# Kernel tuning notes

Measured on AMD Instinct MI355X. Metric: run time of the kernel, lower is better.

## Reference

```python
import jax, jax.numpy as jnp
import numpy as np

H = 16  # hidden_dim
EPS = 1e-5


def _lstm_layer(x, W_ih, W_hh, b_ih, b_hh):
    # x: [B,T,D_in] -> [B,T,H]; PyTorch gate order i,f,g,o
    B = x.shape[0]
    xg = jnp.einsum('btd,gd->btg', x, W_ih) + (b_ih + b_hh)  # [B,T,4H]

    def step(carry, xt):
        h, c = carry
        gates = xt + h @ W_hh.T
        i, f, g, o = jnp.split(gates, 4, axis=-1)
        c = jax.nn.sigmoid(f) * c + jax.nn.sigmoid(i) * jnp.tanh(g)
        h = jax.nn.sigmoid(o) * jnp.tanh(c)
        return (h, c), h

    h0 = jnp.zeros((B, H), x.dtype)
    _, hs = jax.lax.scan(step, (h0, h0), jnp.swapaxes(xg, 0, 1))  # [T,B,H]
    return jnp.swapaxes(hs, 0, 1)


def setup_inputs() -> dict:
    key = jax.random.key(0)
    ks = jax.random.split(key, 20)
    B, T, D, O = 256, 2048, 57, 4
    x = jax.random.normal(ks[0], (B, T, D), dtype=jnp.float32)
    lengths = jnp.maximum(jnp.sort(jax.random.randint(ks[1], (B,), 1, T + 1))[::-1], 1)
    s = 1.0 / np.sqrt(H)
    u = lambda k, shp: jax.random.uniform(k, shp, jnp.float32, -s, s)
    inp = {'x': x, 'lengths': lengths}
    dims_in = [D, H, H]
    for l in range(3):
        inp[f'W_ih{l}'] = u(ks[2 + 4 * l], (4 * H, dims_in[l]))
        inp[f'W_hh{l}'] = u(ks[3 + 4 * l], (4 * H, H))
        inp[f'b_ih{l}'] = u(ks[4 + 4 * l], (4 * H,))
        inp[f'b_hh{l}'] = u(ks[5 + 4 * l], (4 * H,))
    inp['bn_gamma'] = jnp.ones((H,), jnp.float32)
    inp['bn_beta'] = jnp.zeros((H,), jnp.float32)
    inp['fc_w'] = u(ks[14], (O, H))
    inp['fc_b'] = u(ks[15], (O,))
    return inp


def reference(x, lengths, W_ih0, W_hh0, b_ih0, b_hh0, W_ih1, W_hh1, b_ih1, b_hh1,
              W_ih2, W_hh2, b_ih2, b_hh2, bn_gamma, bn_beta, fc_w, fc_b):
    B, T, _ = x.shape
    h = x
    for W_ih, W_hh, b_ih, b_hh in ((W_ih0, W_hh0, b_ih0, b_hh0),
                                    (W_ih1, W_hh1, b_ih1, b_hh1),
                                    (W_ih2, W_hh2, b_ih2, b_hh2)):
        h = _lstm_layer(h, W_ih, W_hh, b_ih, b_hh)
    # pad_packed_sequence: zero out positions past each sequence length
    mask = (jnp.arange(T)[None, :] < lengths[:, None])[:, :, None].astype(h.dtype)
    h = h * mask  # [B,T,H]
    # BatchNorm1d (training mode) over (batch,time) per channel, incl. padding zeros
    mean = jnp.mean(h, axis=(0, 1))
    var = jnp.mean((h - mean) ** 2, axis=(0, 1))
    norm = (h - mean) * jax.lax.rsqrt(var + EPS) * bn_gamma + bn_beta
    return norm @ fc_w.T + fc_b  # [B,T,4]
```

## Files before the change

kernel.cpp:

```cpp
#include <hip/hip_runtime.h>
#include <math.h>

#define TT 2048
#define BBATCH 256
#define DDIM 57
#define NROWS (BBATCH*TT)
#define NF 524288.0f
#define U 8
#define G 4
#define NBUF 8
#define XROWS 64

#define K1 (-1.4426950408889634f)
#define K2 (-2.8853900817779268f)

__device__ __forceinline__ float bcastl(float v, int k) {
  return __uint_as_float((unsigned)__builtin_amdgcn_readlane((int)__float_as_uint(v), k));
}
__device__ __forceinline__ float rcpf(float x) { return __builtin_amdgcn_rcpf(x); }
__device__ __forceinline__ float exp2f_(float x) { return __builtin_amdgcn_exp2f(x); }

template<int PAT>
__device__ __forceinline__ float quadb(float v) {
  return __int_as_float(__builtin_amdgcn_update_dpp(0, __float_as_int(v), PAT, 0xF, 0xF, true));
}

__global__ __launch_bounds__(256) void xg0_gemm_k(
    const float* __restrict__ x, const float* __restrict__ Wih,
    const float* __restrict__ bih, const float* __restrict__ bhh,
    float* __restrict__ xg0)
{
  const int tid = threadIdx.x;
  const int l   = tid & 63;
  const int w   = tid >> 6;
  const int g   = (l & 3) * 16 + (l >> 2);
  const float fac = ((l & 3) == 2) ? K2 : K1;

  __shared__ __align__(16) float xs[XROWS][60];

  float wv[60];
  #pragma unroll
  for (int d = 0; d < 60; ++d) wv[d] = (d < DDIM) ? fac * Wih[g*DDIM + d] : 0.f;
  const float bias = fac * (bih[g] + bhh[g]);

  const int rbase = blockIdx.x * XROWS;
  const float4* xsrc = (const float4*)(x + (size_t)rbase * DDIM);
  #pragma unroll
  for (int it = 0; it < 4; ++it) {
    int i = tid + it*256;
    if (i < 912) {
      float4 v = xsrc[i];
      int f0 = 4*i;
      int r0 = f0/57, d0 = f0 - r0*57;            xs[r0][d0] = v.x;
      int f1 = f0+1, r1 = f1/57, d1 = f1 - r1*57; xs[r1][d1] = v.y;
      int f2 = f0+2, r2 = f2/57, d2 = f2 - r2*57; xs[r2][d2] = v.z;
      int f3 = f0+3, r3 = f3/57, d3 = f3 - r3*57; xs[r3][d3] = v.w;
    }
  }
  if (tid < 192) {
    int r = tid/3, c = 57 + (tid - 3*r);
    xs[r][c] = 0.f;
  }
  __syncthreads();

  #pragma unroll
  for (int rr = 0; rr < 16; ++rr) {
    const int r = w*16 + rr;
    const float4* xr = (const float4*)&xs[r][0];
    float a0 = bias, a1 = 0.f, a2 = 0.f, a3 = 0.f;
    #pragma unroll
    for (int i = 0; i < 15; ++i) {
      float4 v = xr[i];
      a0 += wv[4*i]   * v.x;
      a1 += wv[4*i+1] * v.y;
      a2 += wv[4*i+2] * v.z;
      a3 += wv[4*i+3] * v.w;
    }
    xg0[(size_t)(rbase + r)*64 + l] = (a0 + a1) + (a2 + a3);
  }
}

__global__ __launch_bounds__(192, 1) void lstm_scan_pipe_k(
    const float* __restrict__ xg0,
    const int*   __restrict__ lengths,
    const float* __restrict__ Whh0,
    const float* __restrict__ Wih1, const float* __restrict__ Whh1,
    const float* __restrict__ bih1, const float* __restrict__ bhh1,
    const float* __restrict__ Wih2, const float* __restrict__ Whh2,
    const float* __restrict__ bih2, const float* __restrict__ bhh2,
    float* __restrict__ h2buf, float* __restrict__ partial)
{
  const int tid  = threadIdx.x;
  const int wave = tid >> 6;
  const int lane = tid & 63;
  const int gt   = lane & 3;
  const int ch   = lane >> 2;
  const int g    = gt*16 + ch;
  const int b    = blockIdx.x;
  const int len  = lengths[b];
  const bool isg = (gt == 2);
  const float fac = isg ? K2 : K1;
  const float mg = isg ? (2.f*K2) : 1.f;
  const float ag = isg ? (-K2)    : 0.f;

  __shared__ float lds_h0[NBUF][U][16];
  __shared__ float lds_h1[NBUF][U][16];

  float wa[16], wb[16];
  float bias = 0.f;
  if (wave == 0) {
    #pragma unroll
    for (int k = 0; k < 16; ++k) { wb[k] = fac * Whh0[g*16 + k]; wa[k] = 0.f; }
  } else if (wave == 1) {
    #pragma unroll
    for (int k = 0; k < 16; ++k) { wa[k] = fac * Wih1[g*16 + k]; wb[k] = fac * Whh1[g*16 + k]; }
    bias = fac * (bih1[g] + bhh1[g]);
  } else {
    #pragma unroll
    for (int k = 0; k < 16; ++k) { wa[k] = fac * Wih2[g*16 + k]; wb[k] = fac * Whh2[g*16 + k]; }
    bias = fac * (bih2[g] + bhh2[g]);
  }

  float hs = 0.f, csK = 0.f;
  float sum = 0.f, sq = 0.f;
  const int base = b*TT*64 + lane;
  float* __restrict__ h2row = h2buf + (size_t)b*TT*16;

  auto lstm_update = [&](float dot) {
    float s   = rcpf(1.f + exp2f_(dot));
    float act = fmaf(s, mg, ag);
    float gi = quadb<0x00>(act);
    float gf = quadb<0x55>(act);
    float gg = quadb<0xAA>(act);
    float go = quadb<0xFF>(act);
    float go2 = go + go;
    csK = fmaf(gf, csK, gg * gi);
    float r = rcpf(1.f + exp2f_(csK));
    hs = fmaf(go2, r, -go);
  };
  auto owndot = [&](float seed) {
    float hb[16];
    #pragma unroll
    for (int k = 0; k < 16; ++k) hb[k] = bcastl(hs, 4*k);
    float a0 = seed, a1 = 0.f, a2 = 0.f, a3 = 0.f;
    #pragma unroll
    for (int k = 0; k < 16; k += 4) {
      a0 += wb[k]   * hb[k];
      a1 += wb[k+1] * hb[k+1];
      a2 += wb[k+2] * hb[k+2];
      a3 += wb[k+3] * hb[k+3];
    }
    return (a0 + a1) + (a2 + a3);
  };
  auto indot = [&](const float* hin) {
    float a0 = bias, a1 = 0.f, a2 = 0.f, a3 = 0.f;
    #pragma unroll
    for (int k = 0; k < 16; k += 4) {
      a0 += wa[k]   * hin[k];
      a1 += wa[k+1] * hin[k+1];
      a2 += wa[k+2] * hin[k+2];
      a3 += wa[k+3] * hin[k+3];
    }
    return (a0 + a1) + (a2 + a3);
  };

  const int NS = (len + U - 1) / U;
  const int E  = (NS + 2*G - 1) / G + 1;

  float cur[U], nxt[U];
  if (wave == 0) {
    #pragma unroll
    for (int j = 0; j < U; ++j) cur[j] = xg0[base + j*64];
    #pragma unroll
    for (int j = 0; j < U; ++j) {
      int ip = U + j; ip = ip > TT-1 ? TT-1 : ip;
      nxt[j] = xg0[base + ip*64];
    }
  }

  for (int e = 0; e < E; ++e) {
    #pragma unroll 1
    for (int q = 0; q < G; ++q) {
      const int tw = G*e + q;
      if (wave == 0) {
        const int t = tw;
        if (t < NS) {
          const int p = t & (NBUF-1);
          float ld[U];
          #pragma unroll
          for (int j = 0; j < U; ++j) {
            int ip = (t + 2)*U + j; ip = ip > TT-1 ? TT-1 : ip;
            ld[j] = xg0[base + ip*64];
          }
          #pragma unroll
          for (int j = 0; j < U; ++j) {
            lstm_update(owndot(cur[j]));
            if (gt == 0) lds_h0[p][j][ch] = hs;
          }
          #pragma unroll
          for (int j = 0; j < U; ++j) { cur[j] = nxt[j]; nxt[j] = ld[j]; }
        }
      } else if (wave == 1) {
        const int t = tw - G;
        if (t >= 0 && t < NS) {
          const int p = t & (NBUF-1);
          float xin[U];
          #pragma unroll
          for (int j = 0; j < U; ++j) {
            const float4* hp = (const float4*)&lds_h0[p][j][0];
            float4 h0v = hp[0], h1v = hp[1], h2v = hp[2], h3v = hp[3];
            float hin[16] = {h0v.x,h0v.y,h0v.z,h0v.w, h1v.x,h1v.y,h1v.z,h1v.w,
                             h2v.x,h2v.y,h2v.z,h2v.w, h3v.x,h3v.y,h3v.z,h3v.w};
            xin[j] = indot(hin);
          }
          #pragma unroll
          for (int j = 0; j < U; ++j) {
            lstm_update(owndot(xin[j]));
            if (gt == 0) lds_h1[p][j][ch] = hs;
          }
        }
      } else {
        const int t = tw - 2*G;
        if (t >= 0 && t < NS) {
          const int p = t & (NBUF-1);
          float xin[U];
          #pragma unroll
          for (int j = 0; j < U; ++j) {
            const float4* hp = (const float4*)&lds_h1[p][j][0];
            float4 h0v = hp[0], h1v = hp[1], h2v = hp[2], h3v = hp[3];
            float hin[16] = {h0v.x,h0v.y,h0v.z,h0v.w, h1v.x,h1v.y,h1v.z,h1v.w,
                             h2v.x,h2v.y,h2v.z,h2v.w, h3v.x,h3v.y,h3v.z,h3v.w};
            xin[j] = indot(hin);
          }
          #pragma unroll
          for (int j = 0; j < U; ++j) {
            lstm_update(owndot(xin[j]));
            const int ts = t*U + j;
            if (ts < len) {
              if (gt == 0) h2row[ts*16 + ch] = hs;
              sum += hs; sq += hs*hs;
            }
          }
        }
      }
    }
    __syncthreads();
  }

  for (int idx = len*16 + tid; idx < TT*16; idx += 192)
    h2row[idx] = 0.f;

  if (wave == 2 && gt == 0) {
    partial[b*32 + ch]      = sum;
    partial[b*32 + 16 + ch] = sq;
  }
}

__global__ __launch_bounds__(256) void prep_k(
    const float* __restrict__ partial,
    const float* __restrict__ gamma, const float* __restrict__ beta,
    const float* __restrict__ fcw, const float* __restrict__ fcb,
    float* __restrict__ coef)
{
  const int tid = threadIdx.x;
  const int c = tid & 31, chunk = tid >> 5;
  float acc = 0.f;
  #pragma unroll 8
  for (int bb = 0; bb < 32; ++bb)
    acc += partial[(chunk*32 + bb)*32 + c];
  __shared__ float red[8][32];
  red[chunk][c] = acc;
  __syncthreads();
  if (tid < 32) {
    float tot = 0.f;
    #pragma unroll
    for (int k = 0; k < 8; ++k) tot += red[k][tid];
    red[0][tid] = tot;
  }
  __syncthreads();
  if (tid < 64) {
    const int o = tid >> 4, c2 = tid & 15;
    const float inv_n = 1.0f / NF;
    float mean = red[0][c2] * inv_n;
    float var  = red[0][16 + c2] * inv_n - mean*mean;
    float s  = gamma[c2] * rsqrtf(var + 1e-5f);
    float tb = beta[c2] - mean * s;
    float woc = fcw[o*16 + c2];
    coef[tid] = s * woc;
    float term = tb * woc;
    #pragma unroll
    for (int off = 1; off < 16; off <<= 1) term += __shfl_xor(term, off, 16);
    if (c2 == 0) coef[64 + o] = fcb[o] + term;
  }
}

__global__ __launch_bounds__(256) void finalize_k(
    const float* __restrict__ h2buf, const float* __restrict__ coef,
    float* __restrict__ out)
{
  const int r = blockIdx.x * 256 + threadIdx.x;
  const float4* hp = (const float4*)(h2buf + (size_t)r * 16);
  float4 v0 = hp[0], v1 = hp[1], v2 = hp[2], v3 = hp[3];
  float hv[16] = {v0.x,v0.y,v0.z,v0.w, v1.x,v1.y,v1.z,v1.w,
                  v2.x,v2.y,v2.z,v2.w, v3.x,v3.y,v3.z,v3.w};
  float4 o4;
  float* op = &o4.x;
  #pragma unroll
  for (int o = 0; o < 4; ++o) {
    float a = coef[64 + o];
    #pragma unroll
    for (int c = 0; c < 16; ++c) a += coef[o*16 + c] * hv[c];
    op[o] = a;
  }
  ((float4*)out)[r] = o4;
}

extern "C" void kernel_launch(void* const* d_in, const int* in_sizes, int n_in,
                              void* d_out, int out_size, void* d_ws, size_t ws_size,
                              hipStream_t stream)
{
  const float* x     = (const float*)d_in[0];
  const int* lengths = (const int*)d_in[1];
  const float* W_ih0 = (const float*)d_in[2];
  const float* W_hh0 = (const float*)d_in[3];
  const float* b_ih0 = (const float*)d_in[4];
  const float* b_hh0 = (const float*)d_in[5];
  const float* W_ih1 = (const float*)d_in[6];
  const float* W_hh1 = (const float*)d_in[7];
  const float* b_ih1 = (const float*)d_in[8];
  const float* b_hh1 = (const float*)d_in[9];
  const float* W_ih2 = (const float*)d_in[10];
  const float* W_hh2 = (const float*)d_in[11];
  const float* b_ih2 = (const float*)d_in[12];
  const float* b_hh2 = (const float*)d_in[13];
  const float* gamma = (const float*)d_in[14];
  const float* beta  = (const float*)d_in[15];
  const float* fcw   = (const float*)d_in[16];
  const float* fcb   = (const float*)d_in[17];
  float* out = (float*)d_out;

  float* ws      = (float*)d_ws;
  float* xg0     = ws;
  float* h2      = ws + 33554432;
  float* partial = ws + 33554432 + 8388608;
  float* coef    = partial + 8192;

  hipLaunchKernelGGL(xg0_gemm_k, dim3(NROWS/XROWS), dim3(256), 0, stream,
                     x, W_ih0, b_ih0, b_hh0, xg0);
  hipLaunchKernelGGL(lstm_scan_pipe_k, dim3(256), dim3(192), 0, stream,
                     xg0, lengths, W_hh0, W_ih1, W_hh1, b_ih1, b_hh1,
                     W_ih2, W_hh2, b_ih2, b_hh2, h2, partial);
  hipLaunchKernelGGL(prep_k, dim3(1), dim3(256), 0, stream,
                     partial, gamma, beta, fcw, fcb, coef);
  hipLaunchKernelGGL(finalize_k, dim3(2048), dim3(256), 0, stream, h2, coef, out);
}
```

Before: 646.5 us.

## Fuse LSTM scan, batchnorm stats, and FC epilogue via cooperative grid sync

Merges the scan kernel, the stats-reduction kernel and the finalize kernel into one cooperative launch. Layer-2 hidden states now stay in LDS (32KB per block) instead of going to a global buffer, and each block writes its FC output after a grid-wide sync on the batchnorm partial sums. This removes two kernel launches and the global write and read of the h2 buffer. In exchange it adds a grid barrier, a redundant per-block reduction of all partials, and it depends on all 256 blocks being co-resident.

```diff
diff --git a/kernel.cpp b/kernel.cpp
--- a/kernel.cpp
+++ b/kernel.cpp
@@ -1,5 +1,8 @@
 #include <hip/hip_runtime.h>
+#include <hip/hip_cooperative_groups.h>
 #include <math.h>
+
+namespace cg = cooperative_groups;
 
 #define TT 2048
 #define BBATCH 256
@@ -80,7 +83,7 @@
   }
 }
 
-__global__ __launch_bounds__(192, 1) void lstm_scan_pipe_k(
+__global__ __launch_bounds__(192, 1) void lstm_scan_fused_k(
     const float* __restrict__ xg0,
     const int*   __restrict__ lengths,
     const float* __restrict__ Whh0,
@@ -88,7 +91,9 @@
     const float* __restrict__ bih1, const float* __restrict__ bhh1,
     const float* __restrict__ Wih2, const float* __restrict__ Whh2,
     const float* __restrict__ bih2, const float* __restrict__ bhh2,
-    float* __restrict__ h2buf, float* __restrict__ partial)
+    const float* __restrict__ gamma, const float* __restrict__ beta,
+    const float* __restrict__ fcw, const float* __restrict__ fcb,
+    float* __restrict__ out, float* __restrict__ partial)
 {
   const int tid  = threadIdx.x;
   const int wave = tid >> 6;
@@ -105,6 +110,9 @@
 
   __shared__ float lds_h0[NBUF][U][16];
   __shared__ float lds_h1[NBUF][U][16];
+  __shared__ __align__(16) float lds_h2[TT][16];
+  __shared__ float red[6][32];
+  __shared__ float coef_s[68];
 
   float wa[16], wb[16];
   float bias = 0.f;
@@ -124,7 +132,6 @@
   float hs = 0.f, csK = 0.f;
   float sum = 0.f, sq = 0.f;
   const int base = b*TT*64 + lane;
-  float* __restrict__ h2row = h2buf + (size_t)b*TT*16;
 
   auto lstm_update = [&](float dot) {
     float s   = rcpf(1.f + exp2f_(dot));
@@ -237,7 +244,7 @@
             lstm_update(owndot(xin[j]));
             const int ts = t*U + j;
             if (ts < len) {
-              if (gt == 0) h2row[ts*16 + ch] = hs;
+              if (gt == 0) lds_h2[ts][ch] = hs;
               sum += hs; sq += hs*hs;
             }
           }
@@ -246,35 +253,24 @@
     }
     __syncthreads();
   }
-
-  for (int idx = len*16 + tid; idx < TT*16; idx += 192)
-    h2row[idx] = 0.f;
 
   if (wave == 2 && gt == 0) {
     partial[b*32 + ch]      = sum;
     partial[b*32 + 16 + ch] = sq;
-  }
-}
-
-__global__ __launch_bounds__(256) void prep_k(
-    const float* __restrict__ partial,
-    const float* __restrict__ gamma, const float* __restrict__ beta,
-    const float* __restrict__ fcw, const float* __restrict__ fcb,
-    float* __restrict__ coef)
-{
-  const int tid = threadIdx.x;
+    __threadfence();
+  }
+  cg::this_grid().sync();
+
   const int c = tid & 31, chunk = tid >> 5;
   float acc = 0.f;
-  #pragma unroll 8
-  for (int bb = 0; bb < 32; ++bb)
-    acc += partial[(chunk*32 + bb)*32 + c];
-  __shared__ float red[8][32];
+  for (int bb = chunk; bb < BBATCH; bb += 6)
+    acc += partial[bb*32 + c];
   red[chunk][c] = acc;
   __syncthreads();
   if (tid < 32) {
     float tot = 0.f;
     #pragma unroll
-    for (int k = 0; k < 8; ++k) tot += red[k][tid];
+    for (int k = 0; k < 6; ++k) tot += red[k][tid];
     red[0][tid] = tot;
   }
   __syncthreads();
@@ -283,36 +279,39 @@
     const float inv_n = 1.0f / NF;
     float mean = red[0][c2] * inv_n;
     float var  = red[0][16 + c2] * inv_n - mean*mean;
-    float s  = gamma[c2] * rsqrtf(var + 1e-5f);
-    float tb = beta[c2] - mean * s;
+    float sc = gamma[c2] * rsqrtf(var + 1e-5f);
+    float tb = beta[c2] - mean * sc;
     float woc = fcw[o*16 + c2];
-    coef[tid] = s * woc;
+    coef_s[tid] = sc * woc;
     float term = tb * woc;
     #pragma unroll
     for (int off = 1; off < 16; off <<= 1) term += __shfl_xor(term, off, 16);
-    if (c2 == 0) coef[64 + o] = fcb[o] + term;
-  }
-}
-
-__global__ __launch_bounds__(256) void finalize_k(
-    const float* __restrict__ h2buf, const float* __restrict__ coef,
-    float* __restrict__ out)
-{
-  const int r = blockIdx.x * 256 + threadIdx.x;
-  const float4* hp = (const float4*)(h2buf + (size_t)r * 16);
-  float4 v0 = hp[0], v1 = hp[1], v2 = hp[2], v3 = hp[3];
-  float hv[16] = {v0.x,v0.y,v0.z,v0.w, v1.x,v1.y,v1.z,v1.w,
-                  v2.x,v2.y,v2.z,v2.w, v3.x,v3.y,v3.z,v3.w};
-  float4 o4;
-  float* op = &o4.x;
-  #pragma unroll
-  for (int o = 0; o < 4; ++o) {
-    float a = coef[64 + o];
-    #pragma unroll
-    for (int c = 0; c < 16; ++c) a += coef[o*16 + c] * hv[c];
-    op[o] = a;
-  }
-  ((float4*)out)[r] = o4;
+    if (c2 == 0) coef_s[64 + o] = fcb[o] + term;
+  }
+  __syncthreads();
+
+  float4* outp = (float4*)out + (size_t)b*TT;
+  const float4 bias4 = make_float4(coef_s[64], coef_s[65], coef_s[66], coef_s[67]);
+  for (int t = tid; t < TT; t += 192) {
+    float4 o4;
+    if (t < len) {
+      const float4* hp = (const float4*)&lds_h2[t][0];
+      float4 v0 = hp[0], v1 = hp[1], v2 = hp[2], v3 = hp[3];
+      float hv[16] = {v0.x,v0.y,v0.z,v0.w, v1.x,v1.y,v1.z,v1.w,
+                      v2.x,v2.y,v2.z,v2.w, v3.x,v3.y,v3.z,v3.w};
+      float* op = &o4.x;
+      #pragma unroll
+      for (int o = 0; o < 4; ++o) {
+        float a = coef_s[64 + o];
+        #pragma unroll
+        for (int c3 = 0; c3 < 16; ++c3) a += coef_s[o*16 + c3] * hv[c3];
+        op[o] = a;
+      }
+    } else {
+      o4 = bias4;
+    }
+    outp[t] = o4;
+  }
 }
 
 extern "C" void kernel_launch(void* const* d_in, const int* in_sizes, int n_in,
@@ -341,16 +340,18 @@
 
   float* ws      = (float*)d_ws;
   float* xg0     = ws;
-  float* h2      = ws + 33554432;
-  float* partial = ws + 33554432 + 8388608;
-  float* coef    = partial + 8192;
+  float* partial = ws + 33554432;
 
   hipLaunchKernelGGL(xg0_gemm_k, dim3(NROWS/XROWS), dim3(256), 0, stream,
                      x, W_ih0, b_ih0, b_hh0, xg0);
-  hipLaunchKernelGGL(lstm_scan_pipe_k, dim3(256), dim3(192), 0, stream,
-                     xg0, lengths, W_hh0, W_ih1, W_hh1, b_ih1, b_hh1,
-                     W_ih2, W_hh2, b_ih2, b_hh2, h2, partial);
-  hipLaunchKernelGGL(prep_k, dim3(1), dim3(256), 0, stream,
-                     partial, gamma, beta, fcw, fcb, coef);
-  hipLaunchKernelGGL(finalize_k, dim3(2048), dim3(256), 0, stream, h2, coef, out);
-}
+
+  void* kargs[] = {
+    (void*)&xg0, (void*)&lengths, (void*)&W_hh0,
+    (void*)&W_ih1, (void*)&W_hh1, (void*)&b_ih1, (void*)&b_hh1,
+    (void*)&W_ih2, (void*)&W_hh2, (void*)&b_ih2, (void*)&b_hh2,
+    (void*)&gamma, (void*)&beta, (void*)&fcw, (void*)&fcb,
+    (void*)&out, (void*)&partial
+  };
+  hipLaunchCooperativeKernel((void*)lstm_scan_fused_k, dim3(BBATCH), dim3(192),
+                             kargs, 0, stream);
+}
```

New measurement: 693.4 us. 1.07x slower.
